# Kernel optimization log

Measured on AMD Instinct MI355X. Metric: run time of the kernel, lower is better.

## Reference

```python
import jax, jax.numpy as jnp
import numpy as np

B, H, L, D = 2, 16, 4096, 128
F_DIM = 64          # feature_dim -> phi dim is 2*F_DIM
S_BLK = 64          # block_size
EPS = 1e-6
SCALING = D ** -0.5


def setup_inputs() -> dict:
    key = jax.random.key(0)
    ks = jax.random.split(key, 4)
    return {
        "query_states": jax.random.normal(ks[0], (B, H, L, D), dtype=jnp.float32),
        "key_states": jax.random.normal(ks[1], (B, H, L, D), dtype=jnp.float32),
        "value_states": jax.random.normal(ks[2], (B, H, L, D), dtype=jnp.float32),
        "hedgehog_weights": jax.random.normal(ks[3], (H, D, F_DIM), dtype=jnp.float32),
        "alpha": jnp.float32(4.0),
    }


def _feature_map(x, weights):
    # x: (B,H,N,S,D) -> (B,H,N,S,2F) = cat(softmax(u), softmax(-u))
    u = jnp.einsum('bhnsd,hdf->bhnsf', x, weights)
    return jnp.concatenate([jax.nn.softmax(u, axis=-1),
                            jax.nn.softmax(-u, axis=-1)], axis=-1)


def reference(query_states, key_states, value_states, hedgehog_weights, alpha):
    b, h, l, d = query_states.shape
    n_blocks = l // S_BLK  # L chosen divisible by block_size (no pad path)

    def to_blocks(x):
        return x.reshape(b, h, n_blocks, S_BLK, d)

    q = to_blocks(query_states)
    k = to_blocks(key_states)
    v = to_blocks(value_states)

    phi_q = _feature_map(q, hedgehog_weights)  # (B,H,N,S,2F)
    phi_k = _feature_map(k, hedgehog_weights)

    w = jax.nn.sigmoid(alpha)

    # scan over blocks; carry the running linear-attention state
    def step(carry, inputs):
        S_state, Z_state = carry            # (B,H,2F,D), (B,H,2F)
        pq, pk, qn, kn, vn = inputs         # each (B,H,S,*)
        denom = jnp.maximum(jnp.einsum('bhsf,bhf->bhs', pq, Z_state), EPS)
        linear_out = jnp.einsum('bhsf,bhfd->bhsd', pq, S_state) / denom[..., None]
        S_state = S_state + jnp.einsum('bhsf,bhsd->bhfd', pk, vn)
        Z_state = Z_state + pk.sum(axis=-2)
        scores = jnp.einsum('bhsd,bhtd->bhst', qn, kn) * SCALING
        softmax_out = jnp.einsum('bhst,bhtd->bhsd', jax.nn.softmax(scores, axis=-1), vn)
        out_n = w * softmax_out + (1.0 - w) * linear_out
        return (S_state, Z_state), out_n

    # move block axis to front for scan: (N,B,H,S,*)
    xs = tuple(jnp.moveaxis(a, 2, 0) for a in (phi_q, phi_k, q, k, v))
    S0 = jnp.zeros((b, h, 2 * F_DIM, d), dtype=jnp.float32)
    Z0 = jnp.zeros((b, h, 2 * F_DIM), dtype=jnp.float32)
    _, out_blocks = jax.lax.scan(step, (S0, Z0), xs)  # (N,B,H,S,D)

    out = jnp.moveaxis(out_blocks, 0, 2).reshape(b, h, l, d)
    return out
```

## Files before the change

### kernel.cpp

```cpp
#include <hip/hip_runtime.h>
#include <math.h>

#define B_ 2
#define H_ 16
#define L_ 4096
#define D_ 128
#define F_ 64
#define F2_ 128
#define S_ 64
#define N_ 64
#define BH_ 32
#define NBT_ 2048
#define EPS_ 1e-6f
#define SCALING_ 0.08838834764831845f

typedef float f32x4 __attribute__((ext_vector_type(4)));
typedef short s16x8 __attribute__((ext_vector_type(8)));
typedef short s16x4 __attribute__((ext_vector_type(4)));

#define MFMA(a, b, c) __builtin_amdgcn_mfma_f32_16x16x32_bf16(a, b, c, 0, 0, 0)

__device__ __forceinline__ short f2bf(float f) {
  unsigned u = __float_as_uint(f);
  u += 0x7fffu + ((u >> 16) & 1u);
  return (short)(u >> 16);
}
__device__ __forceinline__ float bf2f(short s) {
  return __uint_as_float(((unsigned)(unsigned short)s) << 16);
}

__device__ __forceinline__ s16x8 frag_f32(const float* p) {
  f32x4 a = *(const f32x4*)p;
  f32x4 b = *(const f32x4*)(p + 4);
  s16x8 r;
  r[0] = f2bf(a[0]); r[1] = f2bf(a[1]); r[2] = f2bf(a[2]); r[3] = f2bf(a[3]);
  r[4] = f2bf(b[0]); r[5] = f2bf(b[1]); r[6] = f2bf(b[2]); r[7] = f2bf(b[3]);
  return r;
}

__device__ __forceinline__ s16x8 swz_frag(const short* base, int row, int rowBytes, int colByte) {
  int byte = row * rowBytes + (colByte ^ ((row & 7) << 4));
  return *(const s16x8*)((const char*)base + byte);
}
__device__ __forceinline__ void lds_w16(short* lds, int row, int rowBytes, int colByte, short v) {
  int byte = row * rowBytes + (colByte ^ ((row & 7) << 4));
  *(short*)((char*)lds + byte) = v;
}

__global__ __launch_bounds__(256)
void prep_w(const float* __restrict__ W, short* __restrict__ Wt)
{
  const int h = blockIdx.x;
  const int tid = threadIdx.x;
  const int f = tid & 63, gq = tid >> 6;
  const float* Wh = W + (size_t)h * D_ * F_;
  short* Wo = Wt + (size_t)h * F_ * D_ + (size_t)f * D_ + gq * 32;
  short buf[32];
#pragma unroll
  for (int j = 0; j < 32; ++j) buf[j] = f2bf(Wh[(size_t)(gq * 32 + j) * F_ + f]);
#pragma unroll
  for (int j2 = 0; j2 < 4; ++j2) {
    s16x8 v;
#pragma unroll
    for (int e = 0; e < 8; ++e) v[e] = buf[j2 * 8 + e];
    *(s16x8*)(Wo + j2 * 8) = v;
  }
}

__global__ __launch_bounds__(256, 3)
void bslh_phase1(const float* __restrict__ K, const float* __restrict__ V,
                 const short* __restrict__ Wt, short* __restrict__ VT,
                 short* __restrict__ dSt, float* __restrict__ dZ)
{
  __shared__ __align__(16) char lds[32 * 1024];
  short* phiT = (short*)lds;
  short* VTs = (short*)(lds + 16384);

  const int blk = blockIdx.x;
  const int bh = blk / N_;
  const int h = bh % H_;
  const int tid = threadIdx.x;
  const int wave = tid >> 6, lane = tid & 63;
  const int rl = lane & 15, g = lane >> 4, kl = g * 8;
  const int r0 = wave * 16;

  {
    const float4* gv = (const float4*)(V + (size_t)blk * S_ * D_);
#pragma unroll
    for (int ii = 0; ii < 8; ++ii) {
      int idx = tid + 256 * ii;
      int s = idx >> 5, c = (idx & 31) * 4;
      float4 v = gv[idx];
      float o0 = __shfl_xor(v.x, 32, 64);
      float o1 = __shfl_xor(v.y, 32, 64);
      float o2 = __shfl_xor(v.z, 32, 64);
      float o3 = __shfl_xor(v.w, 32, 64);
      if (!(tid & 32)) {
        float m[4] = {v.x, v.y, v.z, v.w};
        float o[4] = {o0, o1, o2, o3};
#pragma unroll
        for (int j = 0; j < 4; ++j) {
          int d = c + j;
          unsigned pk = (unsigned)(unsigned short)f2bf(m[j]) |
                        ((unsigned)(unsigned short)f2bf(o[j]) << 16);
          int byte = d * 128 + ((s * 2) ^ ((d & 7) << 4));
          *(unsigned*)((char*)VTs + byte) = pk;
        }
      }
    }
  }

  const float* Kb = K + (size_t)blk * (S_ * D_);
  const short* Wh = Wt + (size_t)h * (F_ * D_);
  const f32x4 z4 = {0.f, 0.f, 0.f, 0.f};

  f32x4 uacc[4] = {z4, z4, z4, z4};
  for (int ks = 0; ks < 4; ++ks) {
    s16x8 a = frag_f32(Kb + (size_t)(r0 + rl) * D_ + ks * 32 + kl);
#pragma unroll
    for (int tn = 0; tn < 4; ++tn) {
      s16x8 b = *(const s16x8*)(Wh + (size_t)(tn * 16 + rl) * D_ + ks * 32 + kl);
      uacc[tn] = MFMA(a, b, uacc[tn]);
    }
  }

#pragma unroll
  for (int reg = 0; reg < 4; ++reg) {
    float mx = -1e30f, mn = 1e30f;
#pragma unroll
    for (int tn = 0; tn < 4; ++tn) {
      mx = fmaxf(mx, uacc[tn][reg]);
      mn = fminf(mn, uacc[tn][reg]);
    }
#pragma unroll
    for (int o = 1; o <= 8; o <<= 1) {
      mx = fmaxf(mx, __shfl_xor(mx, o, 64));
      mn = fminf(mn, __shfl_xor(mn, o, 64));
    }
    float ep[4], em[4], sp = 0.f, sm = 0.f;
#pragma unroll
    for (int tn = 0; tn < 4; ++tn) {
      ep[tn] = __expf(uacc[tn][reg] - mx); sp += ep[tn];
      em[tn] = __expf(mn - uacc[tn][reg]); sm += em[tn];
    }
#pragma unroll
    for (int o = 1; o <= 8; o <<= 1) {
      sp += __shfl_xor(sp, o, 64);
      sm += __shfl_xor(sm, o, 64);
    }
    const float rp = 1.f / sp, rm = 1.f / sm;
    const int srow = r0 + g * 4 + reg;
#pragma unroll
    for (int tn = 0; tn < 4; ++tn) {
      int f = tn * 16 + rl;
      lds_w16(phiT, f,      2 * S_, srow * 2, f2bf(ep[tn] * rp));
      lds_w16(phiT, f + 64, 2 * S_, srow * 2, f2bf(em[tn] * rm));
    }
  }
  __syncthreads();

  {
    float4* dst = (float4*)(VT + (size_t)blk * (D_ * S_));
    const float4* src = (const float4*)VTs;
#pragma unroll
    for (int i = 0; i < 4; ++i) dst[tid + 256 * i] = src[tid + 256 * i];
  }

  {
    const int f = tid >> 1, half = tid & 1;
    float z = 0.f;
#pragma unroll
    for (int j2 = 0; j2 < 4; ++j2) {
      s16x8 v = swz_frag(phiT, f, 2 * S_, (half * 32 + j2 * 8) * 2);
#pragma unroll
      for (int e = 0; e < 8; ++e) z += bf2f(v[e]);
    }
    z += __shfl_xor(z, 1, 64);
    if (half == 0) dZ[(size_t)blk * F2_ + f] = z;
  }

  f32x4 acc[2][8];
#pragma unroll
  for (int tm = 0; tm < 2; ++tm)
#pragma unroll
    for (int tn = 0; tn < 8; ++tn) acc[tm][tn] = z4;

  for (int ks = 0; ks < 2; ++ks) {
    s16x8 a[2];
#pragma unroll
    for (int tm = 0; tm < 2; ++tm)
      a[tm] = swz_frag(VTs, wave * 32 + tm * 16 + rl, 2 * S_, (ks * 32 + kl) * 2);
#pragma unroll
    for (int tn = 0; tn < 8; ++tn) {
      s16x8 b = swz_frag(phiT, tn * 16 + rl, 2 * S_, (ks * 32 + kl) * 2);
#pragma unroll
      for (int tm = 0; tm < 2; ++tm)
        acc[tm][tn] = MFMA(a[tm], b, acc[tm][tn]);
    }
  }
  __syncthreads();

  short* Stb = (short*)lds;
#pragma unroll
  for (int tm = 0; tm < 2; ++tm)
#pragma unroll
    for (int tn = 0; tn < 8; ++tn)
#pragma unroll
      for (int reg = 0; reg < 4; ++reg) {
        float v0 = acc[tm][tn][reg];
        float v1 = __shfl_xor(v0, 1, 64);
        if (!(lane & 1)) {
          int drow = wave * 32 + tm * 16 + g * 4 + reg;
          int fcol = tn * 16 + rl;
          unsigned pk = (unsigned)(unsigned short)f2bf(v0) |
                        ((unsigned)(unsigned short)f2bf(v1) << 16);
          int byte = drow * 256 + ((fcol * 2) ^ ((drow & 7) << 4));
          *(unsigned*)((char*)Stb + byte) = pk;
        }
      }
  __syncthreads();

  float4* dst = (float4*)(dSt + (size_t)blk * (F2_ * D_));
  const float4* srcl = (const float4*)lds;
#pragma unroll
  for (int i = 0; i < 8; ++i) dst[tid + 256 * i] = srcl[tid + 256 * i];
}

__global__ __launch_bounds__(256)
void bslh_scan(short* __restrict__ St, float4* __restrict__ dZ4)
{
  const int tid = threadIdx.x;
  if (blockIdx.x < 512) {
    const int idx = blockIdx.x * 256 + tid;
    const int bh = idx >> 12;
    const int rem = idx & 4095;
    short* p = St + (size_t)bh * N_ * (F2_ * D_) + (size_t)rem * 4;
    float run[4] = {0.f, 0.f, 0.f, 0.f};
    for (int n = 0; n < N_; ++n) {
      s16x4 v = *(const s16x4*)p;
      s16x4 o;
#pragma unroll
      for (int e = 0; e < 4; ++e) {
        o[e] = f2bf(run[e]);
        run[e] += bf2f(v[e]);
      }
      *(s16x4*)p = o;
      p += F2_ * D_;
    }
  } else {
    const int idx = (blockIdx.x - 512) * 256 + tid;
    const int bh = idx >> 5, e = idx & 31;
    float4* p = dZ4 + (size_t)bh * N_ * 32 + e;
    float4 run = make_float4(0.f, 0.f, 0.f, 0.f);
    for (int n = 0; n < N_; ++n) {
      float4 v = p[(size_t)n * 32];
      p[(size_t)n * 32] = run;
      run.x += v.x; run.y += v.y; run.z += v.z; run.w += v.w;
    }
  }
}

__global__ __launch_bounds__(256, 4)
void bslh_phase3(const float* __restrict__ Q, const float* __restrict__ K,
                 const short* __restrict__ VT, const short* __restrict__ Wt,
                 const short* __restrict__ St, const float* __restrict__ Zp,
                 const float* __restrict__ alphap, float* __restrict__ Out)
{
  __shared__ __align__(16) short phi[S_ * F2_];
  __shared__ __align__(16) short Pl[S_ * S_];
  __shared__ float clL[S_];

  const int blk = blockIdx.x;
  const int bh = blk / N_;
  const int h = bh % H_;
  const int tid = threadIdx.x;
  const int wave = tid >> 6, lane = tid & 63;
  const int rl = lane & 15, g = lane >> 4, kl = g * 8;
  const int r0 = wave * 16;

  const short* Sb = St + (size_t)blk * (F2_ * D_);
  const short* VTb = VT + (size_t)blk * (D_ * S_);
  const float* Qb = Q + (size_t)blk * (S_ * D_);
  const float* Kb = K + (size_t)blk * (S_ * D_);
  const short* Wh = Wt + (size_t)h * (F_ * D_);
  const float w = 1.f / (1.f + __expf(-alphap[0]));
  const f32x4 z4 = {0.f, 0.f, 0.f, 0.f};

  s16x8 aq[4];
  f32x4 uacc[4] = {z4, z4, z4, z4};
  for (int ks = 0; ks < 4; ++ks) {
    aq[ks] = frag_f32(Qb + (size_t)(r0 + rl) * D_ + ks * 32 + kl);
#pragma unroll
    for (int tn = 0; tn < 4; ++tn) {
      s16x8 b = *(const s16x8*)(Wh + (size_t)(tn * 16 + rl) * D_ + ks * 32 + kl);
      uacc[tn] = MFMA(aq[ks], b, uacc[tn]);
    }
  }

#pragma unroll
  for (int reg = 0; reg < 4; ++reg) {
    float mx = -1e30f, mn = 1e30f;
#pragma unroll
    for (int tn = 0; tn < 4; ++tn) {
      mx = fmaxf(mx, uacc[tn][reg]);
      mn = fminf(mn, uacc[tn][reg]);
    }
#pragma unroll
    for (int o = 1; o <= 8; o <<= 1) {
      mx = fmaxf(mx, __shfl_xor(mx, o, 64));
      mn = fminf(mn, __shfl_xor(mn, o, 64));
    }
    float ep[4], em[4], sp = 0.f, sm = 0.f;
#pragma unroll
    for (int tn = 0; tn < 4; ++tn) {
      ep[tn] = __expf(uacc[tn][reg] - mx); sp += ep[tn];
      em[tn] = __expf(mn - uacc[tn][reg]); sm += em[tn];
    }
#pragma unroll
    for (int o = 1; o <= 8; o <<= 1) {
      sp += __shfl_xor(sp, o, 64);
      sm += __shfl_xor(sm, o, 64);
    }
    const float rp = 1.f / sp, rm = 1.f / sm;
    const int srow = r0 + g * 4 + reg;
#pragma unroll
    for (int tn = 0; tn < 4; ++tn) {
      int f = tn * 16 + rl;
      lds_w16(phi, srow, 2 * F2_, f * 2,        f2bf(ep[tn] * rp));
      lds_w16(phi, srow, 2 * F2_, (f + 64) * 2, f2bf(em[tn] * rm));
    }
  }
  __syncthreads();

  if (tid < 64) {
    const float* Zb = Zp + (size_t)blk * F2_;
    float den = 0.f;
#pragma unroll
    for (int j2 = 0; j2 < 16; ++j2) {
      s16x8 v = swz_frag(phi, tid, 2 * F2_, j2 * 16);
      f32x4 z0 = *(const f32x4*)(Zb + j2 * 8);
      f32x4 z1 = *(const f32x4*)(Zb + j2 * 8 + 4);
      den += bf2f(v[0]) * z0[0] + bf2f(v[1]) * z0[1] +
             bf2f(v[2]) * z0[2] + bf2f(v[3]) * z0[3] +
             bf2f(v[4]) * z1[0] + bf2f(v[5]) * z1[1] +
             bf2f(v[6]) * z1[2] + bf2f(v[7]) * z1[3];
    }
    clL[tid] = (1.f - w) / fmaxf(den, EPS_);
  }

  f32x4 sacc[4] = {z4, z4, z4, z4};
  for (int ks = 0; ks < 4; ++ks) {
#pragma unroll
    for (int tn = 0; tn < 4; ++tn) {
      s16x8 b = frag_f32(Kb + (size_t)(tn * 16 + rl) * D_ + ks * 32 + kl);
      sacc[tn] = MFMA(aq[ks], b, sacc[tn]);
    }
  }
#pragma unroll
  for (int reg = 0; reg < 4; ++reg) {
    float mx = -1e30f;
#pragma unroll
    for (int tn = 0; tn < 4; ++tn) {
      sacc[tn][reg] *= SCALING_;
      mx = fmaxf(mx, sacc[tn][reg]);
    }
#pragma unroll
    for (int o = 1; o <= 8; o <<= 1) mx = fmaxf(mx, __shfl_xor(mx, o, 64));
    float e_[4], sum = 0.f;
#pragma unroll
    for (int tn = 0; tn < 4; ++tn) {
      e_[tn] = __expf(sacc[tn][reg] - mx);
      sum += e_[tn];
    }
#pragma unroll
    for (int o = 1; o <= 8; o <<= 1) sum += __shfl_xor(sum, o, 64);
    const float pw = w / sum;
    const int srow = r0 + g * 4 + reg;
#pragma unroll
    for (int tn = 0; tn < 4; ++tn)
      lds_w16(Pl, srow, 2 * S_, (tn * 16 + rl) * 2, f2bf(e_[tn] * pw));
  }
  __syncthreads();

  f32x4 acc[8];
#pragma unroll
  for (int tn = 0; tn < 8; ++tn) acc[tn] = z4;

  for (int ks = 0; ks < 4; ++ks) {
    s16x8 a = swz_frag(phi, r0 + rl, 2 * F2_, (ks * 32 + kl) * 2);
#pragma unroll
    for (int tn = 0; tn < 8; ++tn) {
      s16x8 b = swz_frag(Sb, tn * 16 + rl, 2 * F2_, (ks * 32 + kl) * 2);
      acc[tn] = MFMA(a, b, acc[tn]);
    }
  }
  float cl[4];
#pragma unroll
  for (int reg = 0; reg < 4; ++reg) cl[reg] = clL[r0 + g * 4 + reg];
#pragma unroll
  for (int tn = 0; tn < 8; ++tn)
#pragma unroll
    for (int reg = 0; reg < 4; ++reg) acc[tn][reg] *= cl[reg];

  for (int ks = 0; ks < 2; ++ks) {
    s16x8 a = swz_frag(Pl, r0 + rl, 2 * S_, (ks * 32 + kl) * 2);
#pragma unroll
    for (int tn = 0; tn < 8; ++tn) {
      s16x8 b = swz_frag(VTb, tn * 16 + rl, 2 * S_, (ks * 32 + kl) * 2);
      acc[tn] = MFMA(a, b, acc[tn]);
    }
  }

  float* Ob = Out + (size_t)blk * (S_ * D_);
#pragma unroll
  for (int tn = 0; tn < 8; ++tn)
#pragma unroll
    for (int reg = 0; reg < 4; ++reg) {
      int srow = r0 + g * 4 + reg;
      Ob[(size_t)srow * D_ + tn * 16 + rl] = acc[tn][reg];
    }
}

extern "C" void kernel_launch(void* const* d_in, const int* in_sizes, int n_in,
                              void* d_out, int out_size, void* d_ws, size_t ws_size,
                              hipStream_t stream)
{
  const float* Q = (const float*)d_in[0];
  const float* K = (const float*)d_in[1];
  const float* V = (const float*)d_in[2];
  const float* W = (const float*)d_in[3];
  const float* alpha = (const float*)d_in[4];
  float* Out = (float*)d_out;

  short* VT = (short*)d_ws;
  short* St = VT + (size_t)NBT_ * D_ * S_;
  float* dZ = (float*)(St + (size_t)NBT_ * F2_ * D_);
  short* Wt = (short*)(dZ + (size_t)NBT_ * F2_);

  hipLaunchKernelGGL(prep_w, dim3(H_), dim3(256), 0, stream, W, Wt);
  hipLaunchKernelGGL(bslh_phase1, dim3(NBT_), dim3(256), 0, stream,
                     K, V, Wt, VT, St, dZ);
  hipLaunchKernelGGL(bslh_scan, dim3(516), dim3(256), 0, stream, St, (float4*)dZ);
  hipLaunchKernelGGL(bslh_phase3, dim3(NBT_), dim3(256), 0, stream,
                     Q, K, VT, Wt, St, dZ, alpha, Out);
}
```

Before: 172.6 us.

## Cache bf16 K from phase1, store Z in bf16, compute denominator in registers

Phase1 now writes a bf16 copy of K, which phase3 reads instead of re-reading and converting the fp32 K. This halves phase3's K traffic at the cost of an extra 16 MB write in phase1. The Z prefix sums are stored and scanned in bf16 rather than fp32. Phase3 now computes the linear-attention denominator from the fp32 feature values with shuffle reductions, instead of a separate 64-thread LDS pass. That removes a __syncthreads and the clL shared array, but the removed barrier before reading phi/Pl looks risky for cross-wave LDS visibility.

```diff
diff --git a/kernel.cpp b/kernel.cpp
--- a/kernel.cpp
+++ b/kernel.cpp
@@ -70,7 +70,8 @@
 __global__ __launch_bounds__(256, 3)
 void bslh_phase1(const float* __restrict__ K, const float* __restrict__ V,
                  const short* __restrict__ Wt, short* __restrict__ VT,
-                 short* __restrict__ dSt, float* __restrict__ dZ)
+                 short* __restrict__ Kbf, short* __restrict__ dSt,
+                 short* __restrict__ dZ)
 {
   __shared__ __align__(16) char lds[32 * 1024];
   short* phiT = (short*)lds;
@@ -112,11 +113,13 @@
 
   const float* Kb = K + (size_t)blk * (S_ * D_);
   const short* Wh = Wt + (size_t)h * (F_ * D_);
+  short* Ko = Kbf + (size_t)blk * (S_ * D_);
   const f32x4 z4 = {0.f, 0.f, 0.f, 0.f};
 
   f32x4 uacc[4] = {z4, z4, z4, z4};
   for (int ks = 0; ks < 4; ++ks) {
     s16x8 a = frag_f32(Kb + (size_t)(r0 + rl) * D_ + ks * 32 + kl);
+    *(s16x8*)(Ko + (size_t)(r0 + rl) * D_ + ks * 32 + kl) = a;
 #pragma unroll
     for (int tn = 0; tn < 4; ++tn) {
       s16x8 b = *(const s16x8*)(Wh + (size_t)(tn * 16 + rl) * D_ + ks * 32 + kl);
@@ -176,7 +179,7 @@
       for (int e = 0; e < 8; ++e) z += bf2f(v[e]);
     }
     z += __shfl_xor(z, 1, 64);
-    if (half == 0) dZ[(size_t)blk * F2_ + f] = z;
+    if (half == 0) dZ[(size_t)blk * F2_ + f] = f2bf(z);
   }
 
   f32x4 acc[2][8];
@@ -227,7 +230,7 @@
 }
 
 __global__ __launch_bounds__(256)
-void bslh_scan(short* __restrict__ St, float4* __restrict__ dZ4)
+void bslh_scan(short* __restrict__ St, short* __restrict__ dZ)
 {
   const int tid = threadIdx.x;
   if (blockIdx.x < 512) {
@@ -250,25 +253,30 @@
   } else {
     const int idx = (blockIdx.x - 512) * 256 + tid;
     const int bh = idx >> 5, e = idx & 31;
-    float4* p = dZ4 + (size_t)bh * N_ * 32 + e;
-    float4 run = make_float4(0.f, 0.f, 0.f, 0.f);
+    short* p = dZ + (size_t)bh * N_ * F2_ + (size_t)e * 4;
+    float run[4] = {0.f, 0.f, 0.f, 0.f};
     for (int n = 0; n < N_; ++n) {
-      float4 v = p[(size_t)n * 32];
-      p[(size_t)n * 32] = run;
-      run.x += v.x; run.y += v.y; run.z += v.z; run.w += v.w;
+      s16x4 v = *(const s16x4*)p;
+      s16x4 o;
+#pragma unroll
+      for (int e2 = 0; e2 < 4; ++e2) {
+        o[e2] = f2bf(run[e2]);
+        run[e2] += bf2f(v[e2]);
+      }
+      *(s16x4*)p = o;
+      p += F2_;
     }
   }
 }
 
 __global__ __launch_bounds__(256, 4)
-void bslh_phase3(const float* __restrict__ Q, const float* __restrict__ K,
+void bslh_phase3(const float* __restrict__ Q, const short* __restrict__ Kbf,
                  const short* __restrict__ VT, const short* __restrict__ Wt,
-                 const short* __restrict__ St, const float* __restrict__ Zp,
+                 const short* __restrict__ St, const short* __restrict__ Zp,
                  const float* __restrict__ alphap, float* __restrict__ Out)
 {
   __shared__ __align__(16) short phi[S_ * F2_];
   __shared__ __align__(16) short Pl[S_ * S_];
-  __shared__ float clL[S_];
 
   const int blk = blockIdx.x;
   const int bh = blk / N_;
@@ -278,13 +286,21 @@
   const int rl = lane & 15, g = lane >> 4, kl = g * 8;
   const int r0 = wave * 16;
 
+  const float* Qb = Q + (size_t)blk * (S_ * D_);
+  const short* Kb = Kbf + (size_t)blk * (S_ * D_);
   const short* Sb = St + (size_t)blk * (F2_ * D_);
   const short* VTb = VT + (size_t)blk * (D_ * S_);
-  const float* Qb = Q + (size_t)blk * (S_ * D_);
-  const float* Kb = K + (size_t)blk * (S_ * D_);
   const short* Wh = Wt + (size_t)h * (F_ * D_);
+  const short* Zb = Zp + (size_t)blk * F2_;
   const float w = 1.f / (1.f + __expf(-alphap[0]));
   const f32x4 z4 = {0.f, 0.f, 0.f, 0.f};
+
+  float zf0[4], zf1[4];
+#pragma unroll
+  for (int tn = 0; tn < 4; ++tn) {
+    zf0[tn] = bf2f(Zb[tn * 16 + rl]);
+    zf1[tn] = bf2f(Zb[64 + tn * 16 + rl]);
+  }
 
   s16x8 aq[4];
   f32x4 uacc[4] = {z4, z4, z4, z4};
@@ -297,6 +313,16 @@
     }
   }
 
+  f32x4 sacc[4] = {z4, z4, z4, z4};
+  for (int ks = 0; ks < 4; ++ks) {
+#pragma unroll
+    for (int tn = 0; tn < 4; ++tn) {
+      s16x8 b = *(const s16x8*)(Kb + (size_t)(tn * 16 + rl) * D_ + ks * 32 + kl);
+      sacc[tn] = MFMA(aq[ks], b, sacc[tn]);
+    }
+  }
+
+  float cl[4];
 #pragma unroll
   for (int reg = 0; reg < 4; ++reg) {
     float mx = -1e30f, mn = 1e30f;
@@ -323,39 +349,21 @@
     }
     const float rp = 1.f / sp, rm = 1.f / sm;
     const int srow = r0 + g * 4 + reg;
-#pragma unroll
-    for (int tn = 0; tn < 4; ++tn) {
+    float dp = 0.f;
+#pragma unroll
+    for (int tn = 0; tn < 4; ++tn) {
+      float pv = ep[tn] * rp, mv = em[tn] * rm;
+      dp = fmaf(pv, zf0[tn], dp);
+      dp = fmaf(mv, zf1[tn], dp);
       int f = tn * 16 + rl;
-      lds_w16(phi, srow, 2 * F2_, f * 2,        f2bf(ep[tn] * rp));
-      lds_w16(phi, srow, 2 * F2_, (f + 64) * 2, f2bf(em[tn] * rm));
-    }
-  }
-  __syncthreads();
-
-  if (tid < 64) {
-    const float* Zb = Zp + (size_t)blk * F2_;
-    float den = 0.f;
-#pragma unroll
-    for (int j2 = 0; j2 < 16; ++j2) {
-      s16x8 v = swz_frag(phi, tid, 2 * F2_, j2 * 16);
-      f32x4 z0 = *(const f32x4*)(Zb + j2 * 8);
-      f32x4 z1 = *(const f32x4*)(Zb + j2 * 8 + 4);
-      den += bf2f(v[0]) * z0[0] + bf2f(v[1]) * z0[1] +
-             bf2f(v[2]) * z0[2] + bf2f(v[3]) * z0[3] +
-             bf2f(v[4]) * z1[0] + bf2f(v[5]) * z1[1] +
-             bf2f(v[6]) * z1[2] + bf2f(v[7]) * z1[3];
-    }
-    clL[tid] = (1.f - w) / fmaxf(den, EPS_);
-  }
-
-  f32x4 sacc[4] = {z4, z4, z4, z4};
-  for (int ks = 0; ks < 4; ++ks) {
-#pragma unroll
-    for (int tn = 0; tn < 4; ++tn) {
-      s16x8 b = frag_f32(Kb + (size_t)(tn * 16 + rl) * D_ + ks * 32 + kl);
-      sacc[tn] = MFMA(aq[ks], b, sacc[tn]);
-    }
-  }
+      lds_w16(phi, srow, 2 * F2_, f * 2,        f2bf(pv));
+      lds_w16(phi, srow, 2 * F2_, (f + 64) * 2, f2bf(mv));
+    }
+#pragma unroll
+    for (int o = 1; o <= 8; o <<= 1) dp += __shfl_xor(dp, o, 64);
+    cl[reg] = (1.f - w) / fmaxf(dp, EPS_);
+  }
+
 #pragma unroll
   for (int reg = 0; reg < 4; ++reg) {
     float mx = -1e30f;
@@ -380,7 +388,6 @@
     for (int tn = 0; tn < 4; ++tn)
       lds_w16(Pl, srow, 2 * S_, (tn * 16 + rl) * 2, f2bf(e_[tn] * pw));
   }
-  __syncthreads();
 
   f32x4 acc[8];
 #pragma unroll
@@ -394,9 +401,6 @@
       acc[tn] = MFMA(a, b, acc[tn]);
     }
   }
-  float cl[4];
-#pragma unroll
-  for (int reg = 0; reg < 4; ++reg) cl[reg] = clL[r0 + g * 4 + reg];
 #pragma unroll
   for (int tn = 0; tn < 8; ++tn)
 #pragma unroll
@@ -434,13 +438,14 @@
 
   short* VT = (short*)d_ws;
   short* St = VT + (size_t)NBT_ * D_ * S_;
-  float* dZ = (float*)(St + (size_t)NBT_ * F2_ * D_);
-  short* Wt = (short*)(dZ + (size_t)NBT_ * F2_);
+  short* Kbf = St + (size_t)NBT_ * F2_ * D_;
+  short* dZ = Kbf + (size_t)NBT_ * S_ * D_;
+  short* Wt = dZ + (size_t)NBT_ * F2_;
 
   hipLaunchKernelGGL(prep_w, dim3(H_), dim3(256), 0, stream, W, Wt);
   hipLaunchKernelGGL(bslh_phase1, dim3(NBT_), dim3(256), 0, stream,
-                     K, V, Wt, VT, St, dZ);
-  hipLaunchKernelGGL(bslh_scan, dim3(516), dim3(256), 0, stream, St, (float4*)dZ);
+                     K, V, Wt, VT, Kbf, St, dZ);
+  hipLaunchKernelGGL(bslh_scan, dim3(516), dim3(256), 0, stream, St, dZ);
   hipLaunchKernelGGL(bslh_phase3, dim3(NBT_), dim3(256), 0, stream,
-                     Q, K, VT, Wt, St, dZ, alpha, Out);
-}
+                     Q, Kbf, VT, Wt, St, dZ, alpha, Out);
+}
```

Result: slower. 188.0 us (+8.9%).
